# Kernel optimization log

Measured on AMD Instinct MI355X. Metric: run time of the kernel, lower is better.

Reference implementation:

```python
import jax, jax.numpy as jnp
import numpy as np

N = 100000      # nodes
E = 1600000     # edges (avg degree 16)
IN = 128        # in_channels
H = 4           # heads
C = 32          # out_channels per head
NEG_SLOPE = 0.2 # PyG GATConv default


def setup_inputs() -> dict:
    key = jax.random.key(0)
    k = jax.random.split(key, 6)
    x = jax.random.normal(k[0], (N, IN), jnp.float32)
    edge_index = jax.random.randint(k[1], (2, E), 0, N, jnp.int32)
    # Learned params of GATConv: linear weight, per-head attention vectors, bias
    W = jax.random.normal(k[2], (IN, H * C), jnp.float32) / np.sqrt(IN)
    a_src = jax.random.normal(k[3], (H, C), jnp.float32) * 0.1
    a_dst = jax.random.normal(k[4], (H, C), jnp.float32) * 0.1
    bias = jnp.zeros((H * C,), jnp.float32)
    return {"x": x, "edge_index": edge_index, "W": W,
            "a_src": a_src, "a_dst": a_dst, "bias": bias}


def reference(x, edge_index, W, a_src, a_dst, bias):
    n = x.shape[0]
    # Linear transform, per-head view: [N, H, C]
    h = (x @ W).reshape(n, H, C)
    # Node-level attention halves: alpha_i = <h_i, a>  -> [N, H]
    alpha_src = jnp.einsum('nhc,hc->nh', h, a_src)
    alpha_dst = jnp.einsum('nhc,hc->nh', h, a_dst)
    # add_self_loops=True (PyG default)
    loops = jnp.arange(n, dtype=edge_index.dtype)
    src = jnp.concatenate([edge_index[0], loops])  # [E+N]
    dst = jnp.concatenate([edge_index[1], loops])
    # Edge attention logits with LeakyReLU: [E+N, H]
    e = jax.nn.leaky_relu(alpha_src[src] + alpha_dst[dst], NEG_SLOPE)
    # Numerically stable softmax over incoming edges of each destination node
    m = jax.ops.segment_max(e, dst, num_segments=n)          # [N, H]
    e = jnp.exp(e - m[dst])
    denom = jax.ops.segment_sum(e, dst, num_segments=n)      # [N, H]
    att = e / denom[dst]                                     # [E+N, H]
    # Weighted scatter-aggregate of source features: [N, H, C]
    out = jax.ops.segment_sum(att[:, :, None] * h[src], dst, num_segments=n)
    # concat=True: flatten heads, add bias
    return out.reshape(n, H * C) + bias
```

## Files before the change

kernel.cpp:

```cpp
#include <hip/hip_runtime.h>
#include <stdint.h>


#define NBLK 512
#define BKT 64

typedef __bf16 bf16x8 __attribute__((ext_vector_type(8)));
typedef float f32x4 __attribute__((ext_vector_type(4)));

__device__ __forceinline__ float lrelu(float x) { return x >= 0.f ? x : 0.2f * x; }
__device__ __forceinline__ float blo(unsigned u) { return __uint_as_float(u << 16); }
__device__ __forceinline__ float bhi(unsigned u) { return __uint_as_float(u & 0xffff0000u); }

__global__ __launch_bounds__(256) void k_wprep(const float* __restrict__ W, __bf16* __restrict__ Wt) {
  int idx = blockIdx.x * 256 + threadIdx.x;
  int nn = idx & 127, k = idx >> 7;
  Wt[nn * 128 + k] = (__bf16)W[k * 128 + nn];
}

__global__ __launch_bounds__(256) void k_gemm(const float* __restrict__ x, const __bf16* __restrict__ Wt,
                                              const float* __restrict__ a_src, const float* __restrict__ a_dst,
                                              __bf16* __restrict__ h, float* __restrict__ asrc,
                                              float* __restrict__ adst, int n) {
  __shared__ __align__(16) char Wl[32768];
  __shared__ __align__(16) __bf16 hbuf[4][16 * 128];
  int t = threadIdx.x;
  {
    const float4* s4 = (const float4*)Wt;
    for (int i = t; i < 2048; i += 256) {
      int f = i << 4;
      int nr = f >> 8, c = f & 255;
      *(float4*)(Wl + ((nr << 8) | (c ^ ((nr & 7) << 4)))) = s4[i];
    }
  }
  __syncthreads();
  int wv = t >> 6, lane = t & 63;
  int arow = lane & 15, ag = lane >> 4, c15 = lane & 15;
  float as_t[8], ad_t[8];
#pragma unroll
  for (int tile = 0; tile < 8; ++tile) {
    as_t[tile] = a_src[tile * 16 + c15];
    ad_t[tile] = a_dst[tile * 16 + c15];
  }
  int strip = blockIdx.x * 64 + wv * 16;
  int row = strip + arow;
  float4 fa[8];
  if (row < n) {
    const float4* xr = (const float4*)(x + (size_t)row * 128);
#pragma unroll
    for (int q = 0; q < 4; ++q) {
      fa[2 * q]     = xr[q * 8 + ag * 2];
      fa[2 * q + 1] = xr[q * 8 + ag * 2 + 1];
    }
  } else {
#pragma unroll
    for (int q = 0; q < 8; ++q) fa[q] = make_float4(0.f, 0.f, 0.f, 0.f);
  }
  bf16x8 af[4];
#pragma unroll
  for (int q = 0; q < 4; ++q) {
    af[q][0] = (__bf16)fa[2 * q].x;     af[q][1] = (__bf16)fa[2 * q].y;
    af[q][2] = (__bf16)fa[2 * q].z;     af[q][3] = (__bf16)fa[2 * q].w;
    af[q][4] = (__bf16)fa[2 * q + 1].x; af[q][5] = (__bf16)fa[2 * q + 1].y;
    af[q][6] = (__bf16)fa[2 * q + 1].z; af[q][7] = (__bf16)fa[2 * q + 1].w;
  }
  f32x4 acc[8];
#pragma unroll
  for (int tile = 0; tile < 8; ++tile) acc[tile] = (f32x4){0.f, 0.f, 0.f, 0.f};
#pragma unroll
  for (int q = 0; q < 4; ++q) {
    int gb = (q * 64) + (ag << 4);
#pragma unroll
    for (int tile = 0; tile < 8; ++tile) {
      int nn = tile * 16 + c15;
      bf16x8 bf = *(const bf16x8*)(Wl + ((nn << 8) | (gb ^ ((nn & 7) << 4))));
      acc[tile] = __builtin_amdgcn_mfma_f32_16x16x32_bf16(af[q], bf, acc[tile], 0, 0, 0);
    }
  }
#pragma unroll
  for (int hh = 0; hh < 4; ++hh) {
#pragma unroll
    for (int r = 0; r < 4; ++r) {
      float vps = acc[2 * hh][r] * as_t[2 * hh] + acc[2 * hh + 1][r] * as_t[2 * hh + 1];
      float vpd = acc[2 * hh][r] * ad_t[2 * hh] + acc[2 * hh + 1][r] * ad_t[2 * hh + 1];
#pragma unroll
      for (int m = 1; m < 16; m <<= 1) {
        vps += __shfl_xor(vps, m, 64);
        vpd += __shfl_xor(vpd, m, 64);
      }
      if (c15 == 0) {
        int ro = strip + ag * 4 + r;
        if (ro < n) { asrc[ro * 4 + hh] = vps; adst[ro * 4 + hh] = vpd; }
      }
    }
  }
#pragma unroll
  for (int tile = 0; tile < 8; ++tile) {
#pragma unroll
    for (int r = 0; r < 4; ++r)
      hbuf[wv][(ag * 4 + r) * 128 + tile * 16 + c15] = (__bf16)acc[tile][r];
  }
  int rr = lane >> 2, qq = lane & 3;
  int ro = strip + rr;
  if (ro < n) {
    const float4* src = (const float4*)&hbuf[wv][rr * 128 + qq * 32];
    float4* dst = (float4*)(h + (size_t)ro * 128 + qq * 32);
    dst[0] = src[0];
    dst[1] = src[1];
    dst[2] = src[2];
    dst[3] = src[3];
  }
}


__global__ __launch_bounds__(256) void k_hist(const int* __restrict__ ei, int* __restrict__ cnt2,
                                              int e, int NB, int CE) {
  __shared__ int hist[2048];
  int t = threadIdx.x, blk = blockIdx.x;
  for (int j = t; j < NB; j += 256) hist[j] = 0;
  __syncthreads();
  int i0 = blk * CE, i1 = min(e, i0 + CE);
  for (int i = i0 + t; i < i1; i += 256) atomicAdd(&hist[ei[e + i] >> 6], 1);
  __syncthreads();
  for (int j = t; j < NB; j += 256) cnt2[j * NBLK + blk] = hist[j];
}

__global__ __launch_bounds__(256) void k_scanA(int* __restrict__ cnt2, int* __restrict__ bsums, int m) {
  __shared__ int wsum[4];
  int t = threadIdx.x, i = blockIdx.x * 256 + t;
  int wv = t >> 6, lane = t & 63;
  int v = (i < m) ? cnt2[i] : 0;
  int sc = v;
#pragma unroll
  for (int ofs = 1; ofs < 64; ofs <<= 1) {
    int u = __shfl_up(sc, ofs, 64);
    if (lane >= ofs) sc += u;
  }
  if (lane == 63) wsum[wv] = sc;
  __syncthreads();
  int base = 0;
  for (int w = 0; w < wv; ++w) base += wsum[w];
  if (i < m) cnt2[i] = base + sc - v;
  if (t == 255) bsums[blockIdx.x] = base + sc;
}

__global__ __launch_bounds__(256) void k_scanB(int* __restrict__ bsums, int nbs) {
  __shared__ int wsum[4];
  int t = threadIdx.x, wv = t >> 6, lane = t & 63;
  int carry = 0;
  for (int c = 0; c < nbs; c += 256) {
    int i = c + t;
    int v = (i < nbs) ? bsums[i] : 0;
    int sc = v;
#pragma unroll
    for (int ofs = 1; ofs < 64; ofs <<= 1) {
      int u = __shfl_up(sc, ofs, 64);
      if (lane >= ofs) sc += u;
    }
    if (lane == 63) wsum[wv] = sc;
    __syncthreads();
    int base = carry;
    for (int w = 0; w < wv; ++w) base += wsum[w];
    if (i < nbs) bsums[i] = base + sc - v;
    carry += wsum[0] + wsum[1] + wsum[2] + wsum[3];
    __syncthreads();
  }
}

__global__ __launch_bounds__(256) void k_fill2(const int* __restrict__ ei, const int* __restrict__ cnt2,
                                               const int* __restrict__ bsums,
                                               unsigned* __restrict__ ebuf, int e, int NB, int CE) {
  __shared__ int cur[2048];
  int t = threadIdx.x, blk = blockIdx.x;
  for (int j = t; j < NB; j += 256) {
    int idx = j * NBLK + blk;
    cur[j] = cnt2[idx] + bsums[idx >> 8];
  }
  __syncthreads();
  int i0 = blk * CE, i1 = min(e, i0 + CE);
  for (int i = i0 + t; i < i1; i += 256) {
    int s = ei[i], d = ei[e + i];
    int pos = atomicAdd(&cur[d >> 6], 1);
    ebuf[pos] = ((unsigned)(d & 63) << 26) | (unsigned)s;
  }
}

__global__ __launch_bounds__(256) void k_sort(const unsigned* __restrict__ ebuf, const int* __restrict__ cnt2,
                                              const int* __restrict__ bsums,
                                              int* __restrict__ off, int* __restrict__ adj, int n, int NB, int e) {
  __shared__ int lcnt[BKT], lcur[BKT];
  int b = blockIdx.x, t = threadIdx.x;
  int wv = t >> 6, lane = t & 63;
  int i0 = b * NBLK;
  int s0 = cnt2[i0] + bsums[i0 >> 8];
  int s1 = e;
  if (b + 1 < NB) { int i1 = (b + 1) * NBLK; s1 = cnt2[i1] + bsums[i1 >> 8]; }
  int cnt = s1 - s0;
  int d0 = b * BKT;
  if (t < BKT) lcnt[t] = 0;
  __syncthreads();
  for (int j = t; j < cnt; j += 256) atomicAdd(&lcnt[ebuf[s0 + j] >> 26], 1);
  __syncthreads();
  if (wv == 0) {
    int v = lcnt[lane];
    int sc = v;
#pragma unroll
    for (int o = 1; o < 64; o <<= 1) {
      int u = __shfl_up(sc, o, 64);
      if (lane >= o) sc += u;
    }
    lcur[lane] = sc - v;
    if (d0 + lane < n) off[d0 + lane] = s0 + sc - v;
  }
  if (b == 0 && t == 0) off[n] = e;
  __syncthreads();
  for (int j = t; j < cnt; j += 256) {
    unsigned u = ebuf[s0 + j];
    int pos = atomicAdd(&lcur[u >> 26], 1);
    adj[s0 + pos] = (int)(u & 0x03FFFFFFu);
  }
}

__global__ __launch_bounds__(256) void k_gather(const int* __restrict__ adj, const int* __restrict__ off,
                                                const float* __restrict__ asrc, const float* __restrict__ adst,
                                                const unsigned* __restrict__ h32,
                                                const float* __restrict__ bias, float* __restrict__ out, int n) {
  int gid = blockIdx.x * 256 + threadIdx.x;
  int node = gid >> 6, lane = gid & 63;
  if (node >= n) return;
  int head = lane >> 4;
  int o = off[node], oe = off[node + 1];
  float adh = adst[node * 4 + head];
  float ps = __expf(lrelu(asrc[node * 4 + head] + adh));
  unsigned su = h32[((unsigned)node << 6) + lane];
  float acc0 = ps * blo(su), acc1 = ps * bhi(su), dtot = ps;
  int j = o;
  for (; j + 8 <= oe; j += 8) {
    int sv[8];
    unsigned hu[8];
    float av[8];
#pragma unroll
    for (int k = 0; k < 8; ++k) sv[k] = adj[j + k];
#pragma unroll
    for (int k = 0; k < 8; ++k) {
      hu[k] = h32[((unsigned)sv[k] << 6) + lane];
      av[k] = asrc[sv[k] * 4 + head];
    }
#pragma unroll
    for (int k = 0; k < 8; ++k) {
      float p = __expf(lrelu(av[k] + adh));
      dtot += p;
      acc0 += p * blo(hu[k]);
      acc1 += p * bhi(hu[k]);
    }
  }
  for (; j + 2 <= oe; j += 2) {
    int sA = adj[j], sB = adj[j + 1];
    unsigned uA = h32[((unsigned)sA << 6) + lane];
    unsigned uB = h32[((unsigned)sB << 6) + lane];
    float pA = __expf(lrelu(asrc[sA * 4 + head] + adh));
    float pB = __expf(lrelu(asrc[sB * 4 + head] + adh));
    dtot += pA + pB;
    acc0 += pA * blo(uA) + pB * blo(uB);
    acc1 += pA * bhi(uA) + pB * bhi(uB);
  }
  if (j < oe) {
    int s = adj[j];
    unsigned u = h32[((unsigned)s << 6) + lane];
    float p = __expf(lrelu(asrc[s * 4 + head] + adh));
    dtot += p;
    acc0 += p * blo(u);
    acc1 += p * bhi(u);
  }
  float inv = 1.f / dtot;
  float2 bb = ((const float2*)bias)[lane];
  ((float2*)(out + (size_t)node * 128))[lane] = make_float2(acc0 * inv + bb.x, acc1 * inv + bb.y);
}

extern "C" void kernel_launch(void* const* d_in, const int* in_sizes, int n_in,
                              void* d_out, int out_size, void* d_ws, size_t ws_size,
                              hipStream_t stream) {
  const float* x     = (const float*)d_in[0];
  const int*   ei    = (const int*)d_in[1];
  const float* W     = (const float*)d_in[2];
  const float* a_src = (const float*)d_in[3];
  const float* a_dst = (const float*)d_in[4];
  const float* bias  = (const float*)d_in[5];
  float* out = (float*)d_out;

  int n = in_sizes[0] / 128;
  int e = in_sizes[1] / 2;
  int NB = (n + BKT - 1) / BKT;
  int m = NB * NBLK;
  int gridA = (m + 255) / 256;
  int CE = (e + NBLK - 1) / NBLK;

  char* ws = (char*)d_ws;
  size_t ofs = 0;
  auto alloc = [&](size_t bytes) { void* p = ws + ofs; ofs = (ofs + bytes + 15) & ~(size_t)15; return p; };
  __bf16* h      = (__bf16*)alloc((size_t)n * 128 * sizeof(__bf16));
  unsigned* h32  = (unsigned*)h;
  float* asrc    = (float*)alloc((size_t)n * 4 * sizeof(float));
  float* adst    = (float*)alloc((size_t)n * 4 * sizeof(float));
  int* off       = (int*)alloc((size_t)(n + 1) * sizeof(int));
  int* cnt2      = (int*)alloc((size_t)m * sizeof(int));
  int* bsums     = (int*)alloc((size_t)gridA * sizeof(int));
  unsigned* ebuf = (unsigned*)alloc((size_t)e * sizeof(unsigned));
  int* adj       = (int*)alloc((size_t)e * sizeof(int));
  __bf16* Wt     = (__bf16*)alloc((size_t)128 * 128 * sizeof(__bf16));

  hipLaunchKernelGGL(k_wprep, dim3(64), dim3(256), 0, stream, W, Wt);
  hipLaunchKernelGGL(k_gemm, dim3((n + 63) / 64), dim3(256), 0, stream,
                     x, Wt, a_src, a_dst, h, asrc, adst, n);
  hipLaunchKernelGGL(k_hist, dim3(NBLK), dim3(256), 0, stream, ei, cnt2, e, NB, CE);
  hipLaunchKernelGGL(k_scanA, dim3(gridA), dim3(256), 0, stream, cnt2, bsums, m);
  hipLaunchKernelGGL(k_scanB, dim3(1), dim3(256), 0, stream, bsums, gridA);
  hipLaunchKernelGGL(k_fill2, dim3(NBLK), dim3(256), 0, stream, ei, cnt2, bsums, ebuf, e, NB, CE);
  hipLaunchKernelGGL(k_sort, dim3(NB), dim3(256), 0, stream, ebuf, cnt2, bsums, off, adj, n, NB, e);
  hipLaunchKernelGGL(k_gather, dim3((n * 64 + 255) / 256), dim3(256), 0, stream,
                     adj, off, asrc, adst, h32, bias, out, n);
}
```

Before: 179.9 us.

## Fuse CSR build kernels into one cooperative kernel with grid syncs

Merges the weight transpose, histogram, two scan passes, fill and per-bucket sort into a single cooperative launch of 512 blocks separated by grid.sync barriers. This removes five kernel launches and the gaps between them. The sort phase now loops over buckets with a fixed grid instead of one block per bucket, so it has less parallelism. The GEMM epilogue also halves its shared staging buffer by writing h in two halves, which cuts LDS use and may raise occupancy.

```diff
diff --git a/kernel.cpp b/kernel.cpp
--- a/kernel.cpp
+++ b/kernel.cpp
@@ -1,5 +1,8 @@
 #include <hip/hip_runtime.h>
+#include <hip/hip_cooperative_groups.h>
 #include <stdint.h>
+
+namespace cg = cooperative_groups;
 
 
 #define NBLK 512
@@ -12,10 +15,118 @@
 __device__ __forceinline__ float blo(unsigned u) { return __uint_as_float(u << 16); }
 __device__ __forceinline__ float bhi(unsigned u) { return __uint_as_float(u & 0xffff0000u); }
 
-__global__ __launch_bounds__(256) void k_wprep(const float* __restrict__ W, __bf16* __restrict__ Wt) {
-  int idx = blockIdx.x * 256 + threadIdx.x;
-  int nn = idx & 127, k = idx >> 7;
-  Wt[nn * 128 + k] = (__bf16)W[k * 128 + nn];
+__global__ __launch_bounds__(256) void k_coop(const float* __restrict__ W, __bf16* __restrict__ Wt,
+                                              const int* __restrict__ ei, int* __restrict__ cnt2,
+                                              int* __restrict__ bsums, unsigned* __restrict__ ebuf,
+                                              int* __restrict__ off, int* __restrict__ adj,
+                                              int n, int e, int NB, int CE, int nchunk) {
+  cg::grid_group grid = cg::this_grid();
+  __shared__ int smem[2048];
+  __shared__ int wsum[4];
+  int t = threadIdx.x, blk = blockIdx.x;
+  int wv = t >> 6, lane = t & 63;
+  int m = NB * NBLK;
+
+  if (blk < 64) {
+    int idx = blk * 256 + t;
+    int nn = idx & 127, k = idx >> 7;
+    Wt[nn * 128 + k] = (__bf16)W[k * 128 + nn];
+  }
+
+  for (int j = t; j < NB; j += 256) smem[j] = 0;
+  __syncthreads();
+  int i0 = blk * CE, i1 = min(e, i0 + CE);
+  for (int i = i0 + t; i < i1; i += 256) atomicAdd(&smem[ei[e + i] >> 6], 1);
+  __syncthreads();
+  for (int j = t; j < NB; j += 256) cnt2[j * NBLK + blk] = smem[j];
+  grid.sync();
+
+  for (int c = blk; c < nchunk; c += gridDim.x) {
+    int i = c * 256 + t;
+    int v = (i < m) ? cnt2[i] : 0;
+    int sc = v;
+#pragma unroll
+    for (int o = 1; o < 64; o <<= 1) {
+      int u = __shfl_up(sc, o, 64);
+      if (lane >= o) sc += u;
+    }
+    if (lane == 63) wsum[wv] = sc;
+    __syncthreads();
+    int base = 0;
+    for (int w = 0; w < wv; ++w) base += wsum[w];
+    if (i < m) cnt2[i] = base + sc - v;
+    if (t == 255) bsums[c] = base + sc;
+    __syncthreads();
+  }
+  grid.sync();
+
+  if (blk == 0) {
+    int carry = 0;
+    for (int c0 = 0; c0 < nchunk; c0 += 256) {
+      int i = c0 + t;
+      int v = (i < nchunk) ? bsums[i] : 0;
+      int sc = v;
+#pragma unroll
+      for (int o = 1; o < 64; o <<= 1) {
+        int u = __shfl_up(sc, o, 64);
+        if (lane >= o) sc += u;
+      }
+      if (lane == 63) wsum[wv] = sc;
+      __syncthreads();
+      int base = carry;
+      for (int w = 0; w < wv; ++w) base += wsum[w];
+      if (i < nchunk) bsums[i] = base + sc - v;
+      carry += wsum[0] + wsum[1] + wsum[2] + wsum[3];
+      __syncthreads();
+    }
+  }
+  grid.sync();
+
+  for (int j = t; j < NB; j += 256) {
+    int idx = j * NBLK + blk;
+    smem[j] = cnt2[idx] + bsums[idx >> 8];
+  }
+  __syncthreads();
+  for (int i = i0 + t; i < i1; i += 256) {
+    int s = ei[i], d = ei[e + i];
+    int pos = atomicAdd(&smem[d >> 6], 1);
+    ebuf[pos] = ((unsigned)(d & 63) << 26) | (unsigned)s;
+  }
+  grid.sync();
+
+  int* lcnt = smem;
+  int* lcur = smem + 64;
+  for (int b = blk; b < NB; b += gridDim.x) {
+    __syncthreads();
+    int ib = b * NBLK;
+    int s0 = cnt2[ib] + bsums[ib >> 8];
+    int s1 = e;
+    if (b + 1 < NB) { int ib1 = ib + NBLK; s1 = cnt2[ib1] + bsums[ib1 >> 8]; }
+    int cntb = s1 - s0;
+    int d0 = b * BKT;
+    if (t < BKT) lcnt[t] = 0;
+    __syncthreads();
+    for (int j = t; j < cntb; j += 256) atomicAdd(&lcnt[ebuf[s0 + j] >> 26], 1);
+    __syncthreads();
+    if (wv == 0) {
+      int v = lcnt[lane];
+      int sc = v;
+#pragma unroll
+      for (int o = 1; o < 64; o <<= 1) {
+        int u = __shfl_up(sc, o, 64);
+        if (lane >= o) sc += u;
+      }
+      lcur[lane] = sc - v;
+      if (d0 + lane < n) off[d0 + lane] = s0 + sc - v;
+    }
+    __syncthreads();
+    for (int j = t; j < cntb; j += 256) {
+      unsigned u = ebuf[s0 + j];
+      int pos = atomicAdd(&lcur[u >> 26], 1);
+      adj[s0 + pos] = (int)(u & 0x03FFFFFFu);
+    }
+  }
+  if (blk == 0 && t == 0) off[n] = e;
 }
 
 __global__ __launch_bounds__(256) void k_gemm(const float* __restrict__ x, const __bf16* __restrict__ Wt,
@@ -23,7 +134,7 @@
                                               __bf16* __restrict__ h, float* __restrict__ asrc,
                                               float* __restrict__ adst, int n) {
   __shared__ __align__(16) char Wl[32768];
-  __shared__ __align__(16) __bf16 hbuf[4][16 * 128];
+  __shared__ __align__(16) __bf16 hbuf[4][16 * 64];
   int t = threadIdx.x;
   {
     const float4* s4 = (const float4*)Wt;
@@ -94,130 +205,22 @@
       }
     }
   }
-#pragma unroll
-  for (int tile = 0; tile < 8; ++tile) {
-#pragma unroll
-    for (int r = 0; r < 4; ++r)
-      hbuf[wv][(ag * 4 + r) * 128 + tile * 16 + c15] = (__bf16)acc[tile][r];
-  }
   int rr = lane >> 2, qq = lane & 3;
   int ro = strip + rr;
-  if (ro < n) {
-    const float4* src = (const float4*)&hbuf[wv][rr * 128 + qq * 32];
-    float4* dst = (float4*)(h + (size_t)ro * 128 + qq * 32);
-    dst[0] = src[0];
-    dst[1] = src[1];
-    dst[2] = src[2];
-    dst[3] = src[3];
-  }
-}
-
-
-__global__ __launch_bounds__(256) void k_hist(const int* __restrict__ ei, int* __restrict__ cnt2,
-                                              int e, int NB, int CE) {
-  __shared__ int hist[2048];
-  int t = threadIdx.x, blk = blockIdx.x;
-  for (int j = t; j < NB; j += 256) hist[j] = 0;
-  __syncthreads();
-  int i0 = blk * CE, i1 = min(e, i0 + CE);
-  for (int i = i0 + t; i < i1; i += 256) atomicAdd(&hist[ei[e + i] >> 6], 1);
-  __syncthreads();
-  for (int j = t; j < NB; j += 256) cnt2[j * NBLK + blk] = hist[j];
-}
-
-__global__ __launch_bounds__(256) void k_scanA(int* __restrict__ cnt2, int* __restrict__ bsums, int m) {
-  __shared__ int wsum[4];
-  int t = threadIdx.x, i = blockIdx.x * 256 + t;
-  int wv = t >> 6, lane = t & 63;
-  int v = (i < m) ? cnt2[i] : 0;
-  int sc = v;
-#pragma unroll
-  for (int ofs = 1; ofs < 64; ofs <<= 1) {
-    int u = __shfl_up(sc, ofs, 64);
-    if (lane >= ofs) sc += u;
-  }
-  if (lane == 63) wsum[wv] = sc;
-  __syncthreads();
-  int base = 0;
-  for (int w = 0; w < wv; ++w) base += wsum[w];
-  if (i < m) cnt2[i] = base + sc - v;
-  if (t == 255) bsums[blockIdx.x] = base + sc;
-}
-
-__global__ __launch_bounds__(256) void k_scanB(int* __restrict__ bsums, int nbs) {
-  __shared__ int wsum[4];
-  int t = threadIdx.x, wv = t >> 6, lane = t & 63;
-  int carry = 0;
-  for (int c = 0; c < nbs; c += 256) {
-    int i = c + t;
-    int v = (i < nbs) ? bsums[i] : 0;
-    int sc = v;
-#pragma unroll
-    for (int ofs = 1; ofs < 64; ofs <<= 1) {
-      int u = __shfl_up(sc, ofs, 64);
-      if (lane >= ofs) sc += u;
-    }
-    if (lane == 63) wsum[wv] = sc;
-    __syncthreads();
-    int base = carry;
-    for (int w = 0; w < wv; ++w) base += wsum[w];
-    if (i < nbs) bsums[i] = base + sc - v;
-    carry += wsum[0] + wsum[1] + wsum[2] + wsum[3];
-    __syncthreads();
-  }
-}
-
-__global__ __launch_bounds__(256) void k_fill2(const int* __restrict__ ei, const int* __restrict__ cnt2,
-                                               const int* __restrict__ bsums,
-                                               unsigned* __restrict__ ebuf, int e, int NB, int CE) {
-  __shared__ int cur[2048];
-  int t = threadIdx.x, blk = blockIdx.x;
-  for (int j = t; j < NB; j += 256) {
-    int idx = j * NBLK + blk;
-    cur[j] = cnt2[idx] + bsums[idx >> 8];
-  }
-  __syncthreads();
-  int i0 = blk * CE, i1 = min(e, i0 + CE);
-  for (int i = i0 + t; i < i1; i += 256) {
-    int s = ei[i], d = ei[e + i];
-    int pos = atomicAdd(&cur[d >> 6], 1);
-    ebuf[pos] = ((unsigned)(d & 63) << 26) | (unsigned)s;
-  }
-}
-
-__global__ __launch_bounds__(256) void k_sort(const unsigned* __restrict__ ebuf, const int* __restrict__ cnt2,
-                                              const int* __restrict__ bsums,
-                                              int* __restrict__ off, int* __restrict__ adj, int n, int NB, int e) {
-  __shared__ int lcnt[BKT], lcur[BKT];
-  int b = blockIdx.x, t = threadIdx.x;
-  int wv = t >> 6, lane = t & 63;
-  int i0 = b * NBLK;
-  int s0 = cnt2[i0] + bsums[i0 >> 8];
-  int s1 = e;
-  if (b + 1 < NB) { int i1 = (b + 1) * NBLK; s1 = cnt2[i1] + bsums[i1 >> 8]; }
-  int cnt = s1 - s0;
-  int d0 = b * BKT;
-  if (t < BKT) lcnt[t] = 0;
-  __syncthreads();
-  for (int j = t; j < cnt; j += 256) atomicAdd(&lcnt[ebuf[s0 + j] >> 26], 1);
-  __syncthreads();
-  if (wv == 0) {
-    int v = lcnt[lane];
-    int sc = v;
-#pragma unroll
-    for (int o = 1; o < 64; o <<= 1) {
-      int u = __shfl_up(sc, o, 64);
-      if (lane >= o) sc += u;
-    }
-    lcur[lane] = sc - v;
-    if (d0 + lane < n) off[d0 + lane] = s0 + sc - v;
-  }
-  if (b == 0 && t == 0) off[n] = e;
-  __syncthreads();
-  for (int j = t; j < cnt; j += 256) {
-    unsigned u = ebuf[s0 + j];
-    int pos = atomicAdd(&lcur[u >> 26], 1);
-    adj[s0 + pos] = (int)(u & 0x03FFFFFFu);
+#pragma unroll
+  for (int half = 0; half < 2; ++half) {
+#pragma unroll
+    for (int tile = 0; tile < 4; ++tile) {
+#pragma unroll
+      for (int r = 0; r < 4; ++r)
+        hbuf[wv][(ag * 4 + r) * 64 + tile * 16 + c15] = (__bf16)acc[half * 4 + tile][r];
+    }
+    if (ro < n) {
+      const float4* src = (const float4*)&hbuf[wv][rr * 64 + qq * 16];
+      float4* dst = (float4*)(h + (size_t)ro * 128 + half * 64 + qq * 16);
+      dst[0] = src[0];
+      dst[1] = src[1];
+    }
   }
 }
 
@@ -292,7 +295,7 @@
   int e = in_sizes[1] / 2;
   int NB = (n + BKT - 1) / BKT;
   int m = NB * NBLK;
-  int gridA = (m + 255) / 256;
+  int nchunk = (m + 255) / 256;
   int CE = (e + NBLK - 1) / NBLK;
 
   char* ws = (char*)d_ws;
@@ -304,19 +307,17 @@
   float* adst    = (float*)alloc((size_t)n * 4 * sizeof(float));
   int* off       = (int*)alloc((size_t)(n + 1) * sizeof(int));
   int* cnt2      = (int*)alloc((size_t)m * sizeof(int));
-  int* bsums     = (int*)alloc((size_t)gridA * sizeof(int));
+  int* bsums     = (int*)alloc((size_t)nchunk * sizeof(int));
   unsigned* ebuf = (unsigned*)alloc((size_t)e * sizeof(unsigned));
   int* adj       = (int*)alloc((size_t)e * sizeof(int));
   __bf16* Wt     = (__bf16*)alloc((size_t)128 * 128 * sizeof(__bf16));
 
-  hipLaunchKernelGGL(k_wprep, dim3(64), dim3(256), 0, stream, W, Wt);
+  void* args[] = { (void*)&W, (void*)&Wt, (void*)&ei, (void*)&cnt2, (void*)&bsums,
+                   (void*)&ebuf, (void*)&off, (void*)&adj,
+                   (void*)&n, (void*)&e, (void*)&NB, (void*)&CE, (void*)&nchunk };
+  hipLaunchCooperativeKernel((void*)k_coop, dim3(NBLK), dim3(256), args, 0, stream);
   hipLaunchKernelGGL(k_gemm, dim3((n + 63) / 64), dim3(256), 0, stream,
                      x, Wt, a_src, a_dst, h, asrc, adst, n);
-  hipLaunchKernelGGL(k_hist, dim3(NBLK), dim3(256), 0, stream, ei, cnt2, e, NB, CE);
-  hipLaunchKernelGGL(k_scanA, dim3(gridA), dim3(256), 0, stream, cnt2, bsums, m);
-  hipLaunchKernelGGL(k_scanB, dim3(1), dim3(256), 0, stream, bsums, gridA);
-  hipLaunchKernelGGL(k_fill2, dim3(NBLK), dim3(256), 0, stream, ei, cnt2, bsums, ebuf, e, NB, CE);
-  hipLaunchKernelGGL(k_sort, dim3(NB), dim3(256), 0, stream, ebuf, cnt2, bsums, off, adj, n, NB, e);
   hipLaunchKernelGGL(k_gather, dim3((n * 64 + 255) / 256), dim3(256), 0, stream,
                      adj, off, asrc, adst, h32, bias, out, n);
 }
```

Result: slower. 423.8 us (+135.6%).

## Fuse destination histogram into GEMM kernel and shrink staging buffer

Applied to the files above, without the earlier changes.

Merges the edge histogram kernel into the GEMM launch by giving extra blocks a separate histogram branch, so the two independent stages can run concurrently and one launch is removed. NBLK drops from 512 to 128, which makes each histogram block handle more edges and shrinks the count array fed to the scans and fill. The h staging buffer is halved and written out in two passes to cut LDS use and improve occupancy. The histogram reuses the W shared memory region, and the mixed block types may cause load imbalance.

```diff
diff --git a/kernel.cpp b/kernel.cpp
--- a/kernel.cpp
+++ b/kernel.cpp
@@ -2,7 +2,7 @@
 #include <stdint.h>
 
 
-#define NBLK 512
+#define NBLK 128
 #define BKT 64
 
 typedef __bf16 bf16x8 __attribute__((ext_vector_type(8)));
@@ -18,13 +18,28 @@
   Wt[nn * 128 + k] = (__bf16)W[k * 128 + nn];
 }
 
-__global__ __launch_bounds__(256) void k_gemm(const float* __restrict__ x, const __bf16* __restrict__ Wt,
+__global__ __launch_bounds__(256) void k_mega(const float* __restrict__ x, const __bf16* __restrict__ Wt,
                                               const float* __restrict__ a_src, const float* __restrict__ a_dst,
                                               __bf16* __restrict__ h, float* __restrict__ asrc,
-                                              float* __restrict__ adst, int n) {
+                                              float* __restrict__ adst,
+                                              const int* __restrict__ ei, int* __restrict__ cnt2,
+                                              int n, int e, int NB, int CE, int ngb) {
   __shared__ __align__(16) char Wl[32768];
-  __shared__ __align__(16) __bf16 hbuf[4][16 * 128];
+  __shared__ __align__(16) __bf16 hbuf[4][16 * 64];
   int t = threadIdx.x;
+
+  if ((int)blockIdx.x >= ngb) {
+    int hblk = (int)blockIdx.x - ngb;
+    int* hist = (int*)Wl;
+    for (int j = t; j < NB; j += 256) hist[j] = 0;
+    __syncthreads();
+    int i0 = hblk * CE, i1 = min(e, i0 + CE);
+    for (int i = i0 + t; i < i1; i += 256) atomicAdd(&hist[ei[e + i] >> 6], 1);
+    __syncthreads();
+    for (int j = t; j < NB; j += 256) cnt2[j * NBLK + hblk] = hist[j];
+    return;
+  }
+
   {
     const float4* s4 = (const float4*)Wt;
     for (int i = t; i < 2048; i += 256) {
@@ -94,36 +109,25 @@
       }
     }
   }
-#pragma unroll
-  for (int tile = 0; tile < 8; ++tile) {
-#pragma unroll
-    for (int r = 0; r < 4; ++r)
-      hbuf[wv][(ag * 4 + r) * 128 + tile * 16 + c15] = (__bf16)acc[tile][r];
-  }
   int rr = lane >> 2, qq = lane & 3;
   int ro = strip + rr;
-  if (ro < n) {
-    const float4* src = (const float4*)&hbuf[wv][rr * 128 + qq * 32];
-    float4* dst = (float4*)(h + (size_t)ro * 128 + qq * 32);
-    dst[0] = src[0];
-    dst[1] = src[1];
-    dst[2] = src[2];
-    dst[3] = src[3];
-  }
-}
-
-
-__global__ __launch_bounds__(256) void k_hist(const int* __restrict__ ei, int* __restrict__ cnt2,
-                                              int e, int NB, int CE) {
-  __shared__ int hist[2048];
-  int t = threadIdx.x, blk = blockIdx.x;
-  for (int j = t; j < NB; j += 256) hist[j] = 0;
-  __syncthreads();
-  int i0 = blk * CE, i1 = min(e, i0 + CE);
-  for (int i = i0 + t; i < i1; i += 256) atomicAdd(&hist[ei[e + i] >> 6], 1);
-  __syncthreads();
-  for (int j = t; j < NB; j += 256) cnt2[j * NBLK + blk] = hist[j];
-}
+#pragma unroll
+  for (int half = 0; half < 2; ++half) {
+#pragma unroll
+    for (int tile = 0; tile < 4; ++tile) {
+#pragma unroll
+      for (int r = 0; r < 4; ++r)
+        hbuf[wv][(ag * 4 + r) * 64 + tile * 16 + c15] = (__bf16)acc[half * 4 + tile][r];
+    }
+    if (ro < n) {
+      const float4* src = (const float4*)&hbuf[wv][rr * 64 + qq * 16];
+      float4* dst = (float4*)(h + (size_t)ro * 128 + half * 64 + qq * 16);
+      dst[0] = src[0];
+      dst[1] = src[1];
+    }
+  }
+}
+
 
 __global__ __launch_bounds__(256) void k_scanA(int* __restrict__ cnt2, int* __restrict__ bsums, int m) {
   __shared__ int wsum[4];
@@ -291,6 +295,7 @@
   int n = in_sizes[0] / 128;
   int e = in_sizes[1] / 2;
   int NB = (n + BKT - 1) / BKT;
+  int ngb = (n + 63) / 64;
   int m = NB * NBLK;
   int gridA = (m + 255) / 256;
   int CE = (e + NBLK - 1) / NBLK;
@@ -310,9 +315,8 @@
   __bf16* Wt     = (__bf16*)alloc((size_t)128 * 128 * sizeof(__bf16));
 
   hipLaunchKernelGGL(k_wprep, dim3(64), dim3(256), 0, stream, W, Wt);
-  hipLaunchKernelGGL(k_gemm, dim3((n + 63) / 64), dim3(256), 0, stream,
-                     x, Wt, a_src, a_dst, h, asrc, adst, n);
-  hipLaunchKernelGGL(k_hist, dim3(NBLK), dim3(256), 0, stream, ei, cnt2, e, NB, CE);
+  hipLaunchKernelGGL(k_mega, dim3(ngb + NBLK), dim3(256), 0, stream,
+                     x, Wt, a_src, a_dst, h, asrc, adst, ei, cnt2, n, e, NB, CE, ngb);
   hipLaunchKernelGGL(k_scanA, dim3(gridA), dim3(256), 0, stream, cnt2, bsums, m);
   hipLaunchKernelGGL(k_scanB, dim3(1), dim3(256), 0, stream, bsums, gridA);
   hipLaunchKernelGGL(k_fill2, dim3(NBLK), dim3(256), 0, stream, ei, cnt2, bsums, ebuf, e, NB, CE);
```

New measurement: 163.7 us. 9.0% less time.
